# Optimization experiments

Hardware: AMD Instinct MI355X
Metric: run time of the kernel (lower is better)

## Reference

```python
import jax, jax.numpy as jnp
import numpy as np

B, L, D, V = 4096, 200, 64, 100000
ATTR_LEN = (2, 6, 10)  # label_size = 18
NEG = -1e9


def setup_inputs() -> dict:
    key = jax.random.key(0)
    ks = jax.random.split(key, 12)
    x = jax.random.randint(ks[0], (B, L), 0, V)
    lengths = jax.random.randint(ks[1], (B,), 1, L + 1)  # ragged valid lengths >= 1
    x_mask = jnp.arange(L)[None, :] < lengths[:, None]   # prefix-valid bool mask [B,L]
    y = (jax.random.uniform(ks[2], (B, sum(ATTR_LEN))) < 0.5).astype(jnp.float32)
    ob = (jax.random.uniform(ks[3], (B, sum(ATTR_LEN))) < 0.8).astype(jnp.float32)
    emb_table = (jax.random.normal(ks[4], (V, D)) * 0.02).at[0].set(0.0)  # padding_idx=0
    tran_W = jax.random.normal(ks[5], (3, D, D)) * 0.05   # emb_tran Linear weights (per attr)
    tran_b = jnp.zeros((3, D))
    att_W = jax.random.normal(ks[6], (3, D)) * 0.05       # item_att_W: Linear(D,1) per attr
    att_b = jnp.zeros((3,))
    W0 = jax.random.normal(ks[7], (D, ATTR_LEN[0])) * 0.05  # W_all (no bias)
    W1 = jax.random.normal(ks[8], (D, ATTR_LEN[1])) * 0.05
    W2 = jax.random.normal(ks[9], (D, ATTR_LEN[2])) * 0.05
    return {"x": x, "x_mask": x_mask, "y": y, "ob": ob, "emb_table": emb_table,
            "tran_W": tran_W, "tran_b": tran_b, "att_W": att_W, "att_b": att_b,
            "W0": W0, "W1": W1, "W2": W2}


def reference(x, x_mask, y, ob, emb_table, tran_W, tran_b, att_W, att_b, W0, W1, W2):
    # embed: [B,L,D]
    embed = emb_table[x]
    # per-attribute transformed embeddings: [3,B,L,D]
    e = jax.nn.relu(jnp.einsum('bld,ade->able', embed, tran_W) + tran_b[:, None, None, :])
    # attention logits per attribute: [3,B,L]
    att_u = jax.nn.relu(jnp.einsum('able,ae->abl', e, att_W) + att_b[:, None, None])
    # masked softmax over valid prefix (equivalent to the per-sample length loop)
    m = x_mask.astype(e.dtype)
    scores = jnp.where(x_mask[None, :, :], att_u, NEG)
    att = jax.nn.softmax(scores, axis=-1) * m[None, :, :]
    # attention-pooled user representation per attribute: [3,B,D]
    rep = jnp.tanh(jnp.einsum('abl,able->abe', att, e))
    # torch: cat([rep_a.unsqueeze(2)],2).view(B,-1) -> interleaved (d-major, attr-minor) layout
    user_flat = jnp.transpose(rep, (1, 2, 0)).reshape(rep.shape[1], -1)  # [B, 3*D]
    Ddim = emb_table.shape[1]
    W_user = jnp.concatenate([user_flat[:, 0 * Ddim:1 * Ddim] @ W0,
                              user_flat[:, 1 * Ddim:2 * Ddim] @ W1,
                              user_flat[:, 2 * Ddim:3 * Ddim] @ W2], axis=1)
    # W_compact = W_user * ob  (observed-label mask)
    return W_user * ob
```

## Files before the change

### kernel.cpp

```cpp
#include <hip/hip_runtime.h>

typedef unsigned int u32;
typedef unsigned short u16;
typedef unsigned char u8;
typedef unsigned long long u64;

typedef __attribute__((ext_vector_type(8))) short bf16x8;
typedef __attribute__((ext_vector_type(4))) float f32x4;
typedef __attribute__((ext_vector_type(4))) u32 u32x4;

#define L_SEQ 200

__device__ __forceinline__ u16 f2bf(float f) {
    u32 u = __float_as_uint(f);
    return (u16)((u + 0x7FFFu + ((u >> 16) & 1u)) >> 16);
}
__device__ __forceinline__ u32 pk2bf(float fx, float fy) {
    u32 xb = __float_as_uint(fx) + 0x8000u;
    u32 yb = __float_as_uint(fy) + 0x8000u;
    return __byte_perm(xb, yb, 0x7632);
}
__device__ __forceinline__ float wave_sumf(float v) {
#pragma unroll
    for (int off = 32; off; off >>= 1) v += __shfl_xor(v, off, 64);
    return v;
}

__global__ __launch_bounds__(256) void etna_prep(const void* __restrict__ xmask,
                                                 const float* __restrict__ tranW,
                                                 const float* __restrict__ emb,
                                                 void* __restrict__ ws, int Bn, int Vn,
                                                 int doConv) {
    const int tid = threadIdx.x;
    const int bid = blockIdx.x;

    if (doConv) {
        u64* dst = (u64*)((char*)ws + 40960);
        const float4* src = (const float4*)emb;
        int ng = Vn * 16;
        for (int i = bid * 256 + tid; i < ng; i += gridDim.x * 256) {
            float4 v = src[i];
            u64 lo = pk2bf(v.x, v.y);
            u64 hi = pk2bf(v.z, v.w);
            dst[i] = lo | (hi << 32);
        }
    }

    if (bid < 48) {
        int it = bid * 256 + tid;
        int jj = it & 7;
        int ln = (it >> 3) & 63;
        int kh = (it >> 9) & 1;
        int c = (it >> 10) & 3;
        int a = it >> 12;
        int k = kh * 32 + (ln >> 4) * 8 + jj;
        int n = c * 16 + (ln & 15);
        ((u16*)ws)[it] = f2bf(tranW[a * 4096 + k * 64 + n]);
        return;
    }

    const int wv = tid >> 6;
    const int lane = tid & 63;
    int esz;
    {
        u32 accF = 0, acc0 = 0, accO = 0;
#pragma unroll
        for (int k = 0; k < 4; ++k) {
            int i = lane + 64 * k;
            u32 w = (i < 200) ? ((const u32*)xmask)[i] : 0u;
            accF |= (w & 0xFEFEFEFEu);
            acc0 |= (w & 0x000000FFu);
            accO |= (w & 0xFFFFFF00u);
        }
        bool isFloat = __ballot(accF != 0) != 0;
        bool hasB0   = __ballot(acc0 != 0) != 0;
        bool hasOdd  = __ballot(accO != 0) != 0;
        esz = isFloat ? (hasB0 ? 2 : 4) : (hasOdd ? 1 : 4);
    }
    int s = (bid - 48) * 4 + wv;
    if (s < Bn) {
        int len = 0;
        int mbase = s * L_SEQ;
#pragma unroll
        for (int c4 = 0; c4 < 4; ++c4) {
            int l = c4 * 64 + lane;
            bool v = false;
            if (l < L_SEQ) {
                int off = mbase + l;
                if (esz == 1)      v = ((const u8*)xmask)[off] != 0;
                else if (esz == 2) v = ((const u16*)xmask)[off] != 0;
                else               v = ((const u32*)xmask)[off] != 0;
            }
            len += (int)__popcll(__ballot(v));
        }
        if (lane == 0) ((int*)((char*)ws + 24576))[s] = len;
    }
}

template <bool TAB>
__global__ __launch_bounds__(192, 4) void etna_mfma(
    const int* __restrict__ x, const float* __restrict__ ob,
    const float* __restrict__ emb, const float* __restrict__ tranb,
    const float* __restrict__ attW, const float* __restrict__ attb,
    const float* __restrict__ W0, const float* __restrict__ W1,
    const float* __restrict__ W2, float* __restrict__ out,
    const void* __restrict__ ws, int Vn) {
    __shared__ float repl[3][64];

    const int tid = threadIdx.x;
    const int a = tid >> 6;
    const int lane = tid & 63;
    const int col = lane & 15;
    const int g = lane >> 4;
    const int b = blockIdx.x;

    const u16* wsBf = (const u16*)ws;
    bf16x8 Bf[4][2];
#pragma unroll
    for (int c = 0; c < 4; ++c)
#pragma unroll
        for (int kh = 0; kh < 2; ++kh)
            Bf[c][kh] = *(const bf16x8*)&wsBf[(((a * 4 + c) * 2 + kh) * 64 + lane) * 8];

    const int len = ((const int*)((const char*)ws + 24576))[b];
    const u16* wsEmb = (const u16*)((const char*)ws + 40960);

    const float LOG2E = 1.44269504088896f;
    float TB[4], AW[4];
#pragma unroll
    for (int c = 0; c < 4; ++c) {
        TB[c] = tranb[a * 64 + c * 16 + col];
        AW[c] = attW[a * 64 + c * 16 + col] * LOG2E;
    }
    const float AB = attb[a] * LOG2E;

    const int* xrow = x + b * L_SEQ;
    int iv[4];
#pragma unroll
    for (int c4 = 0; c4 < 4; ++c4) {
        int l = c4 * 64 + lane;
        int id = (l < L_SEQ) ? xrow[l] : 0;
        iv[c4] = max(0, min(id, Vn - 1));
    }

    float NUM[4] = {0.f, 0.f, 0.f, 0.f};
    float DEN = 0.f;
    const int ntiles = (len + 15) >> 4;

    auto loadRow = [&](int id, bf16x8& r0, bf16x8& r1) {
        if (TAB) {
            const bf16x8* rp = (const bf16x8*)(wsEmb + (size_t)id * 64);
            r0 = rp[g];
            r1 = rp[4 + g];
        } else {
            const float4* ep4 = (const float4*)(emb + (size_t)id * 64);
            float4 q0 = ep4[2 * g], q1 = ep4[2 * g + 1];
            float4 q2 = ep4[8 + 2 * g], q3 = ep4[9 + 2 * g];
            u32x4 w0, w1;
            w0.x = pk2bf(q0.x, q0.y); w0.y = pk2bf(q0.z, q0.w);
            w0.z = pk2bf(q1.x, q1.y); w0.w = pk2bf(q1.z, q1.w);
            w1.x = pk2bf(q2.x, q2.y); w1.y = pk2bf(q2.z, q2.w);
            w1.z = pk2bf(q3.x, q3.y); w1.w = pk2bf(q3.z, q3.w);
            r0 = __builtin_bit_cast(bf16x8, w0);
            r1 = __builtin_bit_cast(bf16x8, w1);
        }
    };

    bf16x8 a0, a1, n0, n1;
    {
        int p = col;
        int id = __shfl(iv[0], p, 64);
        id = (p < len) ? id : 0;
        loadRow(id, a0, a1);
    }

    for (int t = 0; t < ntiles; ++t) {
        n0 = a0; n1 = a1;
        if (t + 1 < ntiles) {
            int p = (t + 1) * 16 + col;
            int id = __shfl(iv[p >> 6], p & 63, 64);
            id = (p < len) ? id : 0;
            loadRow(id, n0, n1);
        }
        const int l0 = t << 4;

        f32x4 E[4];
#pragma unroll
        for (int c = 0; c < 4; ++c) {
            f32x4 cc = {TB[c], TB[c], TB[c], TB[c]};
            cc = __builtin_amdgcn_mfma_f32_16x16x32_bf16(a0, Bf[c][0], cc, 0, 0, 0);
            cc = __builtin_amdgcn_mfma_f32_16x16x32_bf16(a1, Bf[c][1], cc, 0, 0, 0);
            E[c].x = fmaxf(cc.x, 0.f);
            E[c].y = fmaxf(cc.y, 0.f);
            E[c].z = fmaxf(cc.z, 0.f);
            E[c].w = fmaxf(cc.w, 0.f);
        }
        float p0 = E[0].x * AW[0] + E[1].x * AW[1] + E[2].x * AW[2] + E[3].x * AW[3];
        float p1 = E[0].y * AW[0] + E[1].y * AW[1] + E[2].y * AW[2] + E[3].y * AW[3];
        float p2 = E[0].z * AW[0] + E[1].z * AW[1] + E[2].z * AW[2] + E[3].z * AW[3];
        float p3 = E[0].w * AW[0] + E[1].w * AW[1] + E[2].w * AW[2] + E[3].w * AW[3];
#pragma unroll
        for (int off = 1; off <= 8; off <<= 1) {
            p0 += __shfl_xor(p0, off, 64);
            p1 += __shfl_xor(p1, off, 64);
            p2 += __shfl_xor(p2, off, 64);
            p3 += __shfl_xor(p3, off, 64);
        }
        int lrow = l0 + 4 * g;
        float u0 = fmaxf(p0 + AB, 0.f);
        float u1 = fmaxf(p1 + AB, 0.f);
        float u2 = fmaxf(p2 + AB, 0.f);
        float u3 = fmaxf(p3 + AB, 0.f);
        float s0 = (lrow + 0 < len) ? exp2f(u0) : 0.f;
        float s1 = (lrow + 1 < len) ? exp2f(u1) : 0.f;
        float s2 = (lrow + 2 < len) ? exp2f(u2) : 0.f;
        float s3 = (lrow + 3 < len) ? exp2f(u3) : 0.f;
        DEN += s0 + s1 + s2 + s3;
#pragma unroll
        for (int c = 0; c < 4; ++c)
            NUM[c] += s0 * E[c].x + s1 * E[c].y + s2 * E[c].z + s3 * E[c].w;

        a0 = n0;
        a1 = n1;
    }

    {
        float d = DEN;
        d += __shfl_xor(d, 16, 64);
        d += __shfl_xor(d, 32, 64);
        float rden = 1.0f / fmaxf(d, 1e-20f);
#pragma unroll
        for (int c = 0; c < 4; ++c) {
            float v = NUM[c];
            v += __shfl_xor(v, 16, 64);
            v += __shfl_xor(v, 32, 64);
            if (g == 0) repl[a][c * 16 + col] = tanhf(v * rden);
        }
    }
    __syncthreads();

    if (a == 0) {
        float outv = 0.f;
        {
            int gg = lane; float v = repl[gg % 3][gg / 3];
#pragma unroll
            for (int k = 0; k < 2; ++k) {
                float p = wave_sumf(v * W0[lane * 2 + k]);
                if (lane == k) outv = p;
            }
        }
        {
            int gg = 64 + lane; float v = repl[gg % 3][gg / 3];
#pragma unroll
            for (int k = 0; k < 6; ++k) {
                float p = wave_sumf(v * W1[lane * 6 + k]);
                if (lane == 2 + k) outv = p;
            }
        }
        {
            int gg = 128 + lane; float v = repl[gg % 3][gg / 3];
#pragma unroll
            for (int k = 0; k < 10; ++k) {
                float p = wave_sumf(v * W2[lane * 10 + k]);
                if (lane == 8 + k) outv = p;
            }
        }
        if (lane < 18) out[b * 18 + lane] = outv * ob[b * 18 + lane];
    }
}

extern "C" void kernel_launch(void* const* d_in, const int* in_sizes, int n_in,
                              void* d_out, int out_size, void* d_ws, size_t ws_size,
                              hipStream_t stream) {
    const int* x = (const int*)d_in[0];
    const void* xmask = d_in[1];
    const float* ob = (const float*)d_in[3];
    const float* emb = (const float*)d_in[4];
    const float* tranW = (const float*)d_in[5];
    const float* tranb = (const float*)d_in[6];
    const float* attW = (const float*)d_in[7];
    const float* attb = (const float*)d_in[8];
    const float* W0 = (const float*)d_in[9];
    const float* W1 = (const float*)d_in[10];
    const float* W2 = (const float*)d_in[11];

    const int Bn = in_sizes[0] / L_SEQ;
    const int Vn = in_sizes[4] / 64;

    const size_t need = 40960 + (size_t)Vn * 128;
    const int useTab = (ws_size >= need) ? 1 : 0;

    etna_prep<<<48 + (Bn + 3) / 4, 256, 0, stream>>>(xmask, tranW, emb, d_ws, Bn, Vn, useTab);
    if (useTab)
        etna_mfma<true><<<Bn, 192, 0, stream>>>(x, ob, emb, tranb, attW, attb,
                                                W0, W1, W2, (float*)d_out, d_ws, Vn);
    else
        etna_mfma<false><<<Bn, 192, 0, stream>>>(x, ob, emb, tranb, attW, attb,
                                                 W0, W1, W2, (float*)d_out, d_ws, Vn);
}
```

Measured before the change: 137.0 us.

## Split sequence tiles across two wave halves and use DPP row reductions

Doubles the block to 384 threads so each attribute gets two waves that each process half of the valid sequence tiles, then combines their partial softmax numerators and denominators through shared memory. The intent is to cut the serial per-wave loop length and expose more memory-level parallelism on embedding gathers. It also swaps the 16-lane shuffle reductions for DPP row operations, loads token ids per tile directly instead of preloading and shuffling them, and spreads the final output projection across all six waves. The costs are an extra barrier, more threads per block that may limit occupancy, and redundant weight loads in each wave.

```diff
diff --git a/kernel.cpp b/kernel.cpp
--- a/kernel.cpp
+++ b/kernel.cpp
@@ -20,9 +20,23 @@
     u32 yb = __float_as_uint(fy) + 0x8000u;
     return __byte_perm(xb, yb, 0x7632);
 }
+
+__device__ __forceinline__ float row16_sum(float v) {
+    int x;
+    x = __builtin_amdgcn_update_dpp(0, __float_as_int(v), 0x128, 0xF, 0xF, true);
+    v += __int_as_float(x);
+    x = __builtin_amdgcn_update_dpp(0, __float_as_int(v), 0x124, 0xF, 0xF, true);
+    v += __int_as_float(x);
+    x = __builtin_amdgcn_update_dpp(0, __float_as_int(v), 0x122, 0xF, 0xF, true);
+    v += __int_as_float(x);
+    x = __builtin_amdgcn_update_dpp(0, __float_as_int(v), 0x121, 0xF, 0xF, true);
+    v += __int_as_float(x);
+    return v;
+}
 __device__ __forceinline__ float wave_sumf(float v) {
-#pragma unroll
-    for (int off = 32; off; off >>= 1) v += __shfl_xor(v, off, 64);
+    v = row16_sum(v);
+    v += __shfl_xor(v, 16, 64);
+    v += __shfl_xor(v, 32, 64);
     return v;
 }
 
@@ -98,17 +112,21 @@
 }
 
 template <bool TAB>
-__global__ __launch_bounds__(192, 4) void etna_mfma(
+__global__ __launch_bounds__(384, 4) void etna_mfma(
     const int* __restrict__ x, const float* __restrict__ ob,
     const float* __restrict__ emb, const float* __restrict__ tranb,
     const float* __restrict__ attW, const float* __restrict__ attb,
     const float* __restrict__ W0, const float* __restrict__ W1,
     const float* __restrict__ W2, float* __restrict__ out,
     const void* __restrict__ ws, int Vn) {
+    __shared__ float pN[2][3][64];
+    __shared__ float pD[2][3];
     __shared__ float repl[3][64];
 
     const int tid = threadIdx.x;
-    const int a = tid >> 6;
+    const int w = tid >> 6;
+    const int a = w % 3;
+    const int h = w / 3;
     const int lane = tid & 63;
     const int col = lane & 15;
     const int g = lane >> 4;
@@ -135,17 +153,14 @@
     const float AB = attb[a] * LOG2E;
 
     const int* xrow = x + b * L_SEQ;
-    int iv[4];
-#pragma unroll
-    for (int c4 = 0; c4 < 4; ++c4) {
-        int l = c4 * 64 + lane;
-        int id = (l < L_SEQ) ? xrow[l] : 0;
-        iv[c4] = max(0, min(id, Vn - 1));
-    }
-
-    float NUM[4] = {0.f, 0.f, 0.f, 0.f};
-    float DEN = 0.f;
-    const int ntiles = (len + 15) >> 4;
+
+    auto loadId = [&](int t) -> int {
+        int p = t * 16 + col;
+        int q = (p < L_SEQ) ? p : (L_SEQ - 1);
+        int id = xrow[q];
+        id = max(0, min(id, Vn - 1));
+        return (p < len) ? id : 0;
+    };
 
     auto loadRow = [&](int id, bf16x8& r0, bf16x8& r1) {
         if (TAB) {
@@ -166,23 +181,26 @@
         }
     };
 
-    bf16x8 a0, a1, n0, n1;
-    {
-        int p = col;
-        int id = __shfl(iv[0], p, 64);
-        id = (p < len) ? id : 0;
-        loadRow(id, a0, a1);
-    }
-
-    for (int t = 0; t < ntiles; ++t) {
-        n0 = a0; n1 = a1;
-        if (t + 1 < ntiles) {
-            int p = (t + 1) * 16 + col;
-            int id = __shfl(iv[p >> 6], p & 63, 64);
-            id = (p < len) ? id : 0;
-            loadRow(id, n0, n1);
-        }
-        const int l0 = t << 4;
+    const int nt = (len + 15) >> 4;
+    const int nth = (nt + 1) >> 1;
+    const int tA = h * nth;
+    const int tB = min(nt, tA + nth);
+
+    float NUM[4] = {0.f, 0.f, 0.f, 0.f};
+    float DEN = 0.f;
+
+    bf16x8 a0, a1;
+    int idN = 0;
+    if (tA < tB) {
+        int id0 = loadId(tA);
+        loadRow(id0, a0, a1);
+        idN = loadId(tA + 1);
+    }
+
+    for (int t = tA; t < tB; ++t) {
+        bf16x8 n0 = a0, n1 = a1;
+        if (t + 1 < tB) loadRow(idN, n0, n1);
+        idN = loadId(t + 2);
 
         f32x4 E[4];
 #pragma unroll
@@ -199,14 +217,12 @@
         float p1 = E[0].y * AW[0] + E[1].y * AW[1] + E[2].y * AW[2] + E[3].y * AW[3];
         float p2 = E[0].z * AW[0] + E[1].z * AW[1] + E[2].z * AW[2] + E[3].z * AW[3];
         float p3 = E[0].w * AW[0] + E[1].w * AW[1] + E[2].w * AW[2] + E[3].w * AW[3];
-#pragma unroll
-        for (int off = 1; off <= 8; off <<= 1) {
-            p0 += __shfl_xor(p0, off, 64);
-            p1 += __shfl_xor(p1, off, 64);
-            p2 += __shfl_xor(p2, off, 64);
-            p3 += __shfl_xor(p3, off, 64);
-        }
-        int lrow = l0 + 4 * g;
+        p0 = row16_sum(p0);
+        p1 = row16_sum(p1);
+        p2 = row16_sum(p2);
+        p3 = row16_sum(p3);
+
+        int lrow = (t << 4) + 4 * g;
         float u0 = fmaxf(p0 + AB, 0.f);
         float u1 = fmaxf(p1 + AB, 0.f);
         float u2 = fmaxf(p2 + AB, 0.f);
@@ -228,44 +244,35 @@
         float d = DEN;
         d += __shfl_xor(d, 16, 64);
         d += __shfl_xor(d, 32, 64);
-        float rden = 1.0f / fmaxf(d, 1e-20f);
+        if (lane == 0) pD[h][a] = d;
 #pragma unroll
         for (int c = 0; c < 4; ++c) {
             float v = NUM[c];
             v += __shfl_xor(v, 16, 64);
             v += __shfl_xor(v, 32, 64);
-            if (g == 0) repl[a][c * 16 + col] = tanhf(v * rden);
+            if (g == 0) pN[h][a][c * 16 + col] = v;
         }
     }
     __syncthreads();
 
-    if (a == 0) {
-        float outv = 0.f;
-        {
-            int gg = lane; float v = repl[gg % 3][gg / 3];
-#pragma unroll
-            for (int k = 0; k < 2; ++k) {
-                float p = wave_sumf(v * W0[lane * 2 + k]);
-                if (lane == k) outv = p;
-            }
-        }
-        {
-            int gg = 64 + lane; float v = repl[gg % 3][gg / 3];
-#pragma unroll
-            for (int k = 0; k < 6; ++k) {
-                float p = wave_sumf(v * W1[lane * 6 + k]);
-                if (lane == 2 + k) outv = p;
-            }
-        }
-        {
-            int gg = 128 + lane; float v = repl[gg % 3][gg / 3];
-#pragma unroll
-            for (int k = 0; k < 10; ++k) {
-                float p = wave_sumf(v * W2[lane * 10 + k]);
-                if (lane == 8 + k) outv = p;
-            }
-        }
-        if (lane < 18) out[b * 18 + lane] = outv * ob[b * 18 + lane];
+    if (h == 0) {
+        float dt = pD[0][a] + pD[1][a];
+        float rden = 1.0f / fmaxf(dt, 1e-20f);
+        float nv = pN[0][a][lane] + pN[1][a][lane];
+        repl[a][lane] = tanhf(nv * rden);
+    }
+    __syncthreads();
+
+    {
+        const int AL = (a == 0) ? 2 : (a == 1 ? 6 : 10);
+        const int OFF = (a == 0) ? 0 : (a == 1 ? 2 : 8);
+        const float* Wp = (a == 0) ? W0 : (a == 1 ? W1 : W2);
+        int gg = a * 64 + lane;
+        float v = repl[gg % 3][gg / 3];
+        for (int k = h; k < AL; k += 2) {
+            float pz = wave_sumf(v * Wp[lane * AL + k]);
+            if (lane == 0) out[b * 18 + OFF + k] = pz * ob[b * 18 + OFF + k];
+        }
     }
 }
 
@@ -292,9 +299,9 @@
 
     etna_prep<<<48 + (Bn + 3) / 4, 256, 0, stream>>>(xmask, tranW, emb, d_ws, Bn, Vn, useTab);
     if (useTab)
-        etna_mfma<true><<<Bn, 192, 0, stream>>>(x, ob, emb, tranb, attW, attb,
+        etna_mfma<true><<<Bn, 384, 0, stream>>>(x, ob, emb, tranb, attW, attb,
                                                 W0, W1, W2, (float*)d_out, d_ws, Vn);
     else
-        etna_mfma<false><<<Bn, 192, 0, stream>>>(x, ob, emb, tranb, attW, attb,
+        etna_mfma<false><<<Bn, 384, 0, stream>>>(x, ob, emb, tranb, attW, attb,
                                                  W0, W1, W2, (float*)d_out, d_ws, Vn);
 }
```

Result: slower. 168.9 us (+23.3%).
